# Performance work log

Measured on AMD Instinct MI355X. Metric: run time of the kernel, lower is better.

## Reference

```python
import jax, jax.numpy as jnp
import numpy as np
from jax.scipy.special import logsumexp

B, S, D, T = 32, 512, 768, 9


def setup_inputs() -> dict:
    key = jax.random.key(0)
    ks = jax.random.split(key, 12)
    s = 0.05
    return {
        "x": jax.random.normal(ks[0], (B, S, D), jnp.float32),
        "tags": jax.random.randint(ks[1], (B, S), 0, T, jnp.int32),
        "mask": jnp.ones((B, S), jnp.bool_),
        "w_ih_f": jax.random.normal(ks[2], (4 * D, D), jnp.float32) * s,
        "w_hh_f": jax.random.normal(ks[3], (4 * D, D), jnp.float32) * s,
        "b_f": jnp.zeros((4 * D,), jnp.float32),
        "w_ih_b": jax.random.normal(ks[4], (4 * D, D), jnp.float32) * s,
        "w_hh_b": jax.random.normal(ks[5], (4 * D, D), jnp.float32) * s,
        "b_b": jnp.zeros((4 * D,), jnp.float32),
        "w_cls": jax.random.normal(ks[6], (T, 2 * D), jnp.float32) * s,
        "b_cls": jnp.zeros((T,), jnp.float32),
        "transitions": jax.random.normal(ks[7], (T, T), jnp.float32) * 0.1,
        "start_trans": jax.random.normal(ks[8], (T,), jnp.float32) * 0.1,
        "end_trans": jax.random.normal(ks[9], (T,), jnp.float32) * 0.1,
    }


def _lstm_dir(x, w_ih, w_hh, b):
    # x: [B,S,D] -> hidden states [B,S,H]; PyTorch gate order i,f,g,o.
    Bb, Ss, _ = x.shape
    H = w_hh.shape[1]
    xg = jnp.einsum('bsd,gd->bsg', x, w_ih) + b  # precompute input projections [B,S,4H]

    def step(carry, xg_t):
        h, c = carry
        g = xg_t + h @ w_hh.T
        i, f, gg, o = jnp.split(g, 4, axis=-1)
        c = jax.nn.sigmoid(f) * c + jax.nn.sigmoid(i) * jnp.tanh(gg)
        h = jax.nn.sigmoid(o) * jnp.tanh(c)
        return (h, c), h

    init = (jnp.zeros((Bb, H), x.dtype), jnp.zeros((Bb, H), x.dtype))
    _, hs = jax.lax.scan(step, init, jnp.swapaxes(xg, 0, 1))  # time-major scan
    return jnp.swapaxes(hs, 0, 1)


def _crf_loss(emissions, tags, mask, transitions, start_trans, end_trans):
    # emissions [B,S,T]; negative token-mean log-likelihood (pytorch-crf).
    mf = mask.astype(emissions.dtype)
    # ---- numerator: score of the gold path (fully vectorized) ----
    em = jnp.take_along_axis(emissions, tags[..., None], axis=-1)[..., 0]  # [B,S]
    tr = transitions[tags[:, :-1], tags[:, 1:]]                            # [B,S-1]
    num = start_trans[tags[:, 0]] + em[:, 0]
    num = num + jnp.sum((tr + em[:, 1:]) * mf[:, 1:], axis=1)
    last_idx = jnp.sum(mask.astype(jnp.int32), axis=1) - 1
    last_tags = jnp.take_along_axis(tags, last_idx[:, None], axis=1)[:, 0]
    num = num + end_trans[last_tags]
    # ---- denominator: forward algorithm via scan over time ----
    score0 = start_trans + emissions[:, 0]  # [B,T]

    def step(score, inp):
        em_t, m_t = inp  # [B,T], [B]
        nxt = logsumexp(score[:, :, None] + transitions[None] + em_t[:, None, :], axis=1)
        return jnp.where(m_t[:, None], nxt, score), None

    em_tm = jnp.swapaxes(emissions[:, 1:], 0, 1)  # [S-1,B,T]
    m_tm = jnp.swapaxes(mask[:, 1:], 0, 1)        # [S-1,B]
    score, _ = jax.lax.scan(step, score0, (em_tm, m_tm))
    den = logsumexp(score + end_trans, axis=1)
    llh = num - den
    return -(jnp.sum(llh) / jnp.sum(mf))  # reduction='token_mean', negated


def reference(x, tags, mask, w_ih_f, w_hh_f, b_f, w_ih_b, w_hh_b, b_b,
              w_cls, b_cls, transitions, start_trans, end_trans):
    h_f = _lstm_dir(x, w_ih_f, w_hh_f, b_f)
    h_b = _lstm_dir(x[:, ::-1], w_ih_b, w_hh_b, b_b)[:, ::-1]
    h = jnp.concatenate([h_f, h_b], axis=-1)          # [B,S,2D]
    emissions = h @ w_cls.T + b_cls                   # [B,S,T]
    return _crf_loss(emissions, tags, mask, transitions, start_trans, end_trans)
```

## Files before the change

### kernel.cpp

```cpp
#include <hip/hip_runtime.h>
#include <stdint.h>

#define BB 32
#define SS 512
#define DD 768
#define GG 3072
#define NTAG 9
#define BSR (BB*SS)
#define EMS 12
#define FLS 4
#define NWG 64
#define GR 48

typedef __attribute__((ext_vector_type(8))) short bf16x8;
typedef __attribute__((ext_vector_type(4))) float f32x4;

__device__ __forceinline__ float b2f(unsigned short s) {
    union { unsigned u; float f; } v; v.u = ((unsigned)s) << 16; return v.f;
}
__device__ __forceinline__ unsigned short f2b(float f) {
    union { float f; unsigned u; } v; v.f = f;
    unsigned r = v.u + 0x7FFFu + ((v.u >> 16) & 1u);
    return (unsigned short)(r >> 16);
}
__device__ __forceinline__ int pack2(float a, float b) {
    return (int)f2b(a) | ((int)f2b(b) << 16);
}
__device__ __forceinline__ float sigm_(float x) { return 1.f / (1.f + __expf(-x)); }
__device__ __forceinline__ float tanh_(float x) {
    float e = __expf(2.f * x);
    return 1.f - 2.f / (e + 1.f);
}

__global__ void k_diag(float* out, float v) { out[0] = v; }

__global__ void k_permw(const float* __restrict__ src, unsigned short* __restrict__ dst) {
    int gp = blockIdx.x;
    int g = (gp & 3) * DD + (gp >> 2);
    const float* s = src + (size_t)g * DD;
    unsigned short* d = dst + (size_t)gp * DD;
    for (int j = threadIdx.x; j < DD; j += blockDim.x) d[j] = f2b(s[j]);
}
__global__ void k_permb(const float* __restrict__ src, float* __restrict__ dst) {
    int gp = blockIdx.x * blockDim.x + threadIdx.x;
    if (gp < GG) dst[gp] = src[(gp & 3) * DD + (gp >> 2)];
}

#define BM 128
#define BN 128
#define BK 32
__global__ __launch_bounds__(256, 2) void k_gemm_xg(
    const float* __restrict__ X,
    const unsigned short* __restrict__ Wp,
    const float* __restrict__ bias,
    unsigned short* __restrict__ Xg,
    int rev)
{
    __shared__ unsigned short As[BM * BK];
    __shared__ unsigned short Bs[BN * BK];
    int tid = threadIdx.x;
    int lane = tid & 63, w = tid >> 6;
    int wm = w >> 1, wn = w & 1;
    int rowBase = blockIdx.x * BM;
    int colBase = blockIdx.y * BN;

    f32x4 acc[4][4];
#pragma unroll
    for (int mf = 0; mf < 4; ++mf)
#pragma unroll
        for (int nf = 0; nf < 4; ++nf) { acc[mf][nf][0]=0.f; acc[mf][nf][1]=0.f; acc[mf][nf][2]=0.f; acc[mf][nf][3]=0.f; }

    for (int kt = 0; kt < DD / BK; ++kt) {
#pragma unroll
        for (int c = 0; c < 2; ++c) {
            int id = tid * 2 + c;
            int r = id >> 2, ko = id & 3;
            int rowg = rowBase + r;
            int srow;
            if (rev) { int b = rowg >> 9, t = rowg & 511; srow = b * SS + (SS - 1 - t); }
            else srow = rowg;
            const float* src = X + (size_t)srow * DD + kt * BK + ko * 8;
            float4 v0 = *(const float4*)(src);
            float4 v1 = *(const float4*)(src + 4);
            int blk = ko ^ ((r >> 1) & 3);
            *(int4*)(&As[r * BK + blk * 8]) =
                make_int4(pack2(v0.x, v0.y), pack2(v0.z, v0.w), pack2(v1.x, v1.y), pack2(v1.z, v1.w));
        }
#pragma unroll
        for (int c = 0; c < 2; ++c) {
            int id = tid * 2 + c;
            int r = id >> 2, ko = id & 3;
            int4 v = *(const int4*)(Wp + (size_t)(colBase + r) * DD + kt * BK + ko * 8);
            int blk = ko ^ ((r >> 1) & 3);
            *(int4*)(&Bs[r * BK + blk * 8]) = v;
        }
        __syncthreads();
        bf16x8 af[4], bfr[4];
        int ko = lane >> 4;
#pragma unroll
        for (int mf = 0; mf < 4; ++mf) {
            int r = wm * 64 + mf * 16 + (lane & 15);
            af[mf] = *(const bf16x8*)(&As[r * BK + (ko ^ ((r >> 1) & 3)) * 8]);
        }
#pragma unroll
        for (int nf = 0; nf < 4; ++nf) {
            int r = wn * 64 + nf * 16 + (lane & 15);
            bfr[nf] = *(const bf16x8*)(&Bs[r * BK + (ko ^ ((r >> 1) & 3)) * 8]);
        }
#pragma unroll
        for (int mf = 0; mf < 4; ++mf)
#pragma unroll
            for (int nf = 0; nf < 4; ++nf)
                acc[mf][nf] = __builtin_amdgcn_mfma_f32_16x16x32_bf16(af[mf], bfr[nf], acc[mf][nf], 0, 0, 0);
        __syncthreads();
    }
#pragma unroll
    for (int mf = 0; mf < 4; ++mf)
#pragma unroll
        for (int nf = 0; nf < 4; ++nf) {
            int colg = colBase + wn * 64 + nf * 16 + (lane & 15);
            float bv = bias[colg];
#pragma unroll
            for (int i = 0; i < 4; ++i) {
                int rowg = rowBase + wm * 64 + mf * 16 + (lane >> 4) * 4 + i;
                Xg[(size_t)rowg * GG + colg] = f2b(acc[mf][nf][i] + bv);
            }
        }
}

__global__ __launch_bounds__(384, 1) void k_lstm(
    const unsigned short* __restrict__ xg_f, const unsigned short* __restrict__ xg_b,
    const unsigned short* __restrict__ whh_f, const unsigned short* __restrict__ whh_b,
    unsigned short* __restrict__ hs_f, unsigned short* __restrict__ hs_b,
    unsigned int* __restrict__ flags,
    unsigned int* __restrict__ done)
{
    int bid = blockIdx.x;

    if (bid >= 2 * NWG) {
        int dir = bid - 2 * NWG;
        if (threadIdx.x >= 64) return;
        int lane = threadIdx.x;
        const unsigned int* flg = flags + (size_t)dir * SS * 64 * FLS;
        unsigned int* dn = done + (size_t)dir * SS * 128;
        for (int t = 0; t < SS - 1; ++t) {
            const unsigned int* fp = flg + (size_t)t * 64 * FLS + lane * FLS;
            while (__hip_atomic_load(fp, __ATOMIC_RELAXED, __HIP_MEMORY_SCOPE_AGENT) == 0u)
                __builtin_amdgcn_s_sleep(1);
            if (lane < 4)
                __hip_atomic_store(dn + (size_t)t * 128 + lane * 32, 1u,
                                   __ATOMIC_RELAXED, __HIP_MEMORY_SCOPE_AGENT);
        }
        return;
    }

    int dir = bid >> 6;
    int wg = bid & 63;
    const unsigned short* xg = dir ? xg_b : xg_f;
    const unsigned short* whh = dir ? whh_b : whh_f;
    unsigned short* hs = dir ? hs_b : hs_f;
    unsigned int* flgD = flags + (size_t)dir * SS * 64 * FLS;
    const unsigned int* dnD = done + (size_t)dir * SS * 128 + (wg & 3) * 32;

    int tid = threadIdx.x;
    int lane = tid & 63, w = tid >> 6;
    int mt = w >> 1, nt = w & 1;
    int g0 = wg * GR;
    int ko = lane >> 4;

    int wrow = g0 + mt * 16 + (lane & 15);
    bf16x8 wf[24];
#pragma unroll
    for (int kt = 0; kt < 24; ++kt)
        wf[kt] = *(const bf16x8*)(whh + (size_t)wrow * DD + kt * 32 + ko * 8);

    int bcol = nt * 16 + (lane & 15);
    int g4 = wg * 12 + mt * 4;
    int gp4 = g0 + mt * 16 + ko * 4;
    const unsigned short* xgrow = xg + (size_t)bcol * SS * GG + gp4;
    unsigned short* hrow = hs + (size_t)bcol * SS * DD;
    float c = 0.f;

    short4 xv = *(const short4*)xgrow;
    for (int t = 0; t < SS; ++t) {
        f32x4 acc;
        acc[0] = b2f((unsigned short)xv.x);
        acc[1] = b2f((unsigned short)xv.y);
        acc[2] = b2f((unsigned short)xv.z);
        acc[3] = b2f((unsigned short)xv.w);
        if (t > 0) {
            const unsigned short* hb = hrow + (size_t)(t - 1) * DD + ko * 8;
#pragma unroll
            for (int kt = 0; kt < 24; ++kt) {
                bf16x8 hv = *(const bf16x8*)(hb + kt * 32);
                acc = __builtin_amdgcn_mfma_f32_16x16x32_bf16(wf[kt], hv, acc, 0, 0, 0);
            }
        }
        float si = sigm_(acc[0]);
        float sf = sigm_(acc[1]);
        float tg = tanh_(acc[2]);
        float so = sigm_(acc[3]);
        c = sf * c + si * tg;
        float h = so * tanh_(c);

        unsigned short hb16 = f2b(h);
        unsigned short pb16 = (unsigned short)__shfl_xor((int)hb16, 16, 64);
        unsigned hp = (unsigned)hb16 | ((unsigned)pb16 << 16);
        unsigned hp2 = (unsigned)__shfl_xor((int)hp, 32, 64);
        if (ko == 0) {
            unsigned long long v8 = ((unsigned long long)hp2 << 32) | (unsigned long long)hp;
            __hip_atomic_store((unsigned long long*)(hrow + (size_t)t * DD + g4), v8,
                               __ATOMIC_RELAXED, __HIP_MEMORY_SCOPE_AGENT);
        }

        if (t == SS - 1) break;

        asm volatile("s_waitcnt vmcnt(0)" ::: "memory");
        __syncthreads();
        if (tid == 0)
            __hip_atomic_store(flgD + (size_t)t * 64 * FLS + wg * FLS, 1u,
                               __ATOMIC_RELAXED, __HIP_MEMORY_SCOPE_AGENT);

        xv = *(const short4*)(xgrow + (size_t)(t + 1) * GG);

        while (__hip_atomic_load(dnD + (size_t)t * 128, __ATOMIC_RELAXED, __HIP_MEMORY_SCOPE_AGENT) == 0)
            __builtin_amdgcn_s_sleep(1);
        asm volatile("" ::: "memory");
    }
}

__global__ void k_emis(const unsigned short* __restrict__ hs_f, const unsigned short* __restrict__ hs_b,
                       const float* __restrict__ wcls, const float* __restrict__ bcls,
                       float* __restrict__ em)
{
    int row = blockIdx.x * 4 + (threadIdx.x >> 6);
    int lane = threadIdx.x & 63;
    int b = row >> 9, t = row & 511;
    const unsigned long long* hfq = (const unsigned long long*)(hs_f + (size_t)row * DD);
    const unsigned long long* hbq = (const unsigned long long*)(hs_b + ((size_t)(b * SS + (SS - 1 - t))) * DD);
    float p[NTAG];
#pragma unroll
    for (int tau = 0; tau < NTAG; ++tau) p[tau] = 0.f;
#pragma unroll
    for (int it = 0; it < 3; ++it) {
        int j4 = lane + it * 64;
        unsigned long long af = hfq[j4];
        unsigned long long ab = hbq[j4];
#pragma unroll
        for (int e = 0; e < 4; ++e) {
            int j = j4 * 4 + e;
            float hv  = b2f((unsigned short)(af >> (16 * e)));
            float hv2 = b2f((unsigned short)(ab >> (16 * e)));
#pragma unroll
            for (int tau = 0; tau < NTAG; ++tau) {
                p[tau] += hv * wcls[tau * 2 * DD + j];
                p[tau] += hv2 * wcls[tau * 2 * DD + DD + j];
            }
        }
    }
#pragma unroll
    for (int tau = 0; tau < NTAG; ++tau) {
        float v = p[tau];
        for (int m = 32; m; m >>= 1) v += __shfl_xor(v, m, 64);
        if (lane == 0) em[(size_t)row * EMS + tau] = v + bcls[tau];
    }
}

__global__ void k_crf(const float* __restrict__ em, const int* __restrict__ tags,
                      const float* __restrict__ trans, const float* __restrict__ start_t,
                      const float* __restrict__ end_t, float* __restrict__ llh)
{
    int b = blockIdx.x;
    int lane = threadIdx.x;
    const int* tg = tags + b * SS;
    const float* emb = em + (size_t)b * SS * EMS;

    float np = 0.f;
    for (int it = 0; it < 8; ++it) {
        int t = 1 + lane + it * 64;
        if (t < SS) {
            int t0 = tg[t - 1], t1 = tg[t];
            np += trans[t0 * NTAG + t1] + emb[t * EMS + t1];
        }
    }
    for (int m = 32; m; m >>= 1) np += __shfl_xor(np, m, 64);

    float score, ec;
    float tc[NTAG];
    if (lane < NTAG) {
        score = start_t[lane] + emb[lane];
        ec = end_t[lane];
#pragma unroll
        for (int i = 0; i < NTAG; ++i) tc[i] = trans[i * NTAG + lane];
    } else {
        score = -1e30f; ec = 0.f;
#pragma unroll
        for (int i = 0; i < NTAG; ++i) tc[i] = 0.f;
    }
    int eidx = (lane < NTAG) ? lane : 0;
    for (int t = 1; t < SS; ++t) {
        float vv[NTAG];
        float mx = -1e30f;
#pragma unroll
        for (int i = 0; i < NTAG; ++i) {
            float si = __shfl(score, i, 64);
            vv[i] = si + tc[i];
            mx = fmaxf(mx, vv[i]);
        }
        float sum = 0.f;
#pragma unroll
        for (int i = 0; i < NTAG; ++i) sum += __expf(vv[i] - mx);
        float ns = mx + __logf(sum) + emb[t * EMS + eidx];
        score = (lane < NTAG) ? ns : -1e30f;
    }
    float sv = (lane < NTAG) ? score + ec : -1e30f;
    float mx = sv;
    for (int m = 32; m; m >>= 1) mx = fmaxf(mx, __shfl_xor(mx, m, 64));
    float se = (lane < NTAG) ? __expf(sv - mx) : 0.f;
    for (int m = 32; m; m >>= 1) se += __shfl_xor(se, m, 64);
    float den = mx + __logf(se);
    if (lane == 0) {
        float num = np + start_t[tg[0]] + emb[tg[0]] + end_t[tg[SS - 1]];
        llh[b] = num - den;
    }
}

__global__ void k_loss(const float* __restrict__ llh, float* __restrict__ out) {
    int lane = threadIdx.x;
    float v = (lane < BB) ? llh[lane] : 0.f;
    for (int m = 32; m; m >>= 1) v += __shfl_xor(v, m, 64);
    if (lane == 0) out[0] = -v / (float)(BB * SS);
}

extern "C" void kernel_launch(void* const* d_in, const int* in_sizes, int n_in,
                              void* d_out, int out_size, void* d_ws, size_t ws_size,
                              hipStream_t stream) {
    (void)in_sizes; (void)n_in; (void)out_size;
    const float* x      = (const float*)d_in[0];
    const int* tags     = (const int*)d_in[1];
    const float* wihF   = (const float*)d_in[3];
    const float* whhF   = (const float*)d_in[4];
    const float* bF     = (const float*)d_in[5];
    const float* wihB   = (const float*)d_in[6];
    const float* whhB   = (const float*)d_in[7];
    const float* bBi    = (const float*)d_in[8];
    const float* wcls   = (const float*)d_in[9];
    const float* bcls   = (const float*)d_in[10];
    const float* trans  = (const float*)d_in[11];
    const float* startT = (const float*)d_in[12];
    const float* endT   = (const float*)d_in[13];
    float* out = (float*)d_out;

    const size_t szW  = (size_t)GG * DD * 2;
    const size_t szB  = GG * 4;
    const size_t szXg = (size_t)BSR * GG * 2;
    const size_t szHs = (size_t)BB * SS * DD * 2;
    const size_t szEm = (size_t)BSR * EMS * 4;
    const size_t szFl = (size_t)2 * SS * 64 * FLS * 4;
    const size_t szDn = (size_t)2 * SS * 128 * 4;
    const size_t NEED = 3*szW + 2*szB + 2*szXg + 2*szHs + szEm + 256 + szFl + szDn + 4096;

    if (ws_size < NEED) {
        k_diag<<<1, 1, 0, stream>>>(out, (float)(ws_size >> 20));
        return;
    }

    char* wp = (char*)d_ws;
    auto alloc = [&](size_t bytes) { char* p = wp; wp += (bytes + 255) & ~(size_t)255; return p; };
    unsigned short* whhFp = (unsigned short*)alloc(szW);
    unsigned short* whhBp = (unsigned short*)alloc(szW);
    unsigned short* wihP  = (unsigned short*)alloc(szW);
    float* bFp = (float*)alloc(szB);
    float* bBp = (float*)alloc(szB);
    unsigned short* hsF = (unsigned short*)alloc(szHs);
    unsigned short* hsB = (unsigned short*)alloc(szHs);
    float* em  = (float*)alloc(szEm);
    float* llh = (float*)alloc(256);
    unsigned int* flags = (unsigned int*)alloc(szFl);
    unsigned int* done  = (unsigned int*)alloc(szDn);
    unsigned short* xgF = (unsigned short*)alloc(szXg);
    unsigned short* xgB = (unsigned short*)alloc(szXg);

    k_permw<<<GG, 256, 0, stream>>>(whhF, whhFp);
    k_permw<<<GG, 256, 0, stream>>>(whhB, whhBp);
    k_permb<<<GG / 256, 256, 0, stream>>>(bF, bFp);
    k_permb<<<GG / 256, 256, 0, stream>>>(bBi, bBp);
    hipMemsetAsync(flags, 0, szFl, stream);
    hipMemsetAsync(done, 0, szDn, stream);

    dim3 gg(BSR / BM, GG / BN);
    k_permw<<<GG, 256, 0, stream>>>(wihF, wihP);
    k_gemm_xg<<<gg, 256, 0, stream>>>(x, wihP, bFp, xgF, 0);
    k_permw<<<GG, 256, 0, stream>>>(wihB, wihP);
    k_gemm_xg<<<gg, 256, 0, stream>>>(x, wihP, bBp, xgB, 1);

    k_lstm<<<2 * NWG + 2, 384, 0, stream>>>(xgF, xgB, whhFp, whhBp, hsF, hsB, flags, done);

    k_emis<<<BSR / 4, 256, 0, stream>>>(hsF, hsB, wcls, bcls, em);
    k_crf<<<BB, 64, 0, stream>>>(em, tags, trans, startT, endT, llh);
    k_loss<<<1, 64, 0, stream>>>(llh, out);
}
```

Before: 3.761 ms.

## Speculatively prefetch LSTM hidden state before barrier, validate via sentinel fill

```diff
diff --git a/kernel.cpp b/kernel.cpp
--- a/kernel.cpp
+++ b/kernel.cpp
@@ -11,6 +11,7 @@
 #define FLS 4
 #define NWG 64
 #define GR 48
+#define SENT 0xFFFFFFFFFFFFFFFFULL
 
 typedef __attribute__((ext_vector_type(8))) short bf16x8;
 typedef __attribute__((ext_vector_type(4))) float f32x4;
@@ -154,6 +155,7 @@
         return;
     }
 
+    __shared__ int stoken;
     int dir = bid >> 6;
     int wg = bid & 63;
     const unsigned short* xg = dir ? xg_b : xg_f;
@@ -167,6 +169,7 @@
     int mt = w >> 1, nt = w & 1;
     int g0 = wg * GR;
     int ko = lane >> 4;
+    if (tid == 0) stoken = -1;
 
     int wrow = g0 + mt * 16 + (lane & 15);
     bf16x8 wf[24];
@@ -180,7 +183,9 @@
     const unsigned short* xgrow = xg + (size_t)bcol * SS * GG + gp4;
     unsigned short* hrow = hs + (size_t)bcol * SS * DD;
     float c = 0.f;
-
+    __syncthreads();
+
+    unsigned long long va[24], vb[24];
     short4 xv = *(const short4*)xgrow;
     for (int t = 0; t < SS; ++t) {
         f32x4 acc;
@@ -189,11 +194,11 @@
         acc[2] = b2f((unsigned short)xv.z);
         acc[3] = b2f((unsigned short)xv.w);
         if (t > 0) {
-            const unsigned short* hb = hrow + (size_t)(t - 1) * DD + ko * 8;
 #pragma unroll
             for (int kt = 0; kt < 24; ++kt) {
-                bf16x8 hv = *(const bf16x8*)(hb + kt * 32);
-                acc = __builtin_amdgcn_mfma_f32_16x16x32_bf16(wf[kt], hv, acc, 0, 0, 0);
+                union { unsigned long long q2[2]; bf16x8 h8; } u;
+                u.q2[0] = va[kt]; u.q2[1] = vb[kt];
+                acc = __builtin_amdgcn_mfma_f32_16x16x32_bf16(wf[kt], u.h8, acc, 0, 0, 0);
             }
         }
         float si = sigm_(acc[0]);
@@ -223,9 +228,39 @@
 
         xv = *(const short4*)(xgrow + (size_t)(t + 1) * GG);
 
-        while (__hip_atomic_load(dnD + (size_t)t * 128, __ATOMIC_RELAXED, __HIP_MEMORY_SCOPE_AGENT) == 0)
+        const unsigned long long* qb =
+            (const unsigned long long*)(hrow + (size_t)t * DD) + ko * 2;
+#pragma unroll
+        for (int kt = 0; kt < 24; ++kt) {
+            va[kt] = qb[kt * 8];
+            vb[kt] = qb[kt * 8 + 1];
+        }
+
+        if (w == 0) {
+            while (__hip_atomic_load(dnD + (size_t)t * 128, __ATOMIC_RELAXED, __HIP_MEMORY_SCOPE_AGENT) == 0)
+                __builtin_amdgcn_s_sleep(1);
+            if (lane == 0)
+                __hip_atomic_store(&stoken, t, __ATOMIC_RELEASE, __HIP_MEMORY_SCOPE_WORKGROUP);
+        }
+        while (__hip_atomic_load(&stoken, __ATOMIC_ACQUIRE, __HIP_MEMORY_SCOPE_WORKGROUP) < t)
             __builtin_amdgcn_s_sleep(1);
-        asm volatile("" ::: "memory");
+
+        for (;;) {
+            int nbad = 0;
+#pragma unroll
+            for (int kt = 0; kt < 24; ++kt) {
+                if (va[kt] == SENT) {
+                    va[kt] = __hip_atomic_load(qb + kt * 8, __ATOMIC_RELAXED, __HIP_MEMORY_SCOPE_AGENT);
+                    nbad += (va[kt] == SENT);
+                }
+                if (vb[kt] == SENT) {
+                    vb[kt] = __hip_atomic_load(qb + kt * 8 + 1, __ATOMIC_RELAXED, __HIP_MEMORY_SCOPE_AGENT);
+                    nbad += (vb[kt] == SENT);
+                }
+            }
+            if (!nbad) break;
+            __builtin_amdgcn_s_sleep(1);
+        }
     }
 }
 
@@ -387,6 +422,8 @@
     k_permb<<<GG / 256, 256, 0, stream>>>(bBi, bBp);
     hipMemsetAsync(flags, 0, szFl, stream);
     hipMemsetAsync(done, 0, szDn, stream);
+    hipMemsetAsync(hsF, 0xFF, szHs, stream);
+    hipMemsetAsync(hsB, 0xFF, szHs, stream);
 
     dim3 gg(BSR / BM, GG / BN);
     k_permw<<<GG, 256, 0, stream>>>(wihF, wihP);
```

Result: slower. 6.179 ms (+64.3%).
